# Performance work log

Measured on AMD Instinct MI355X. Metric: run time of the kernel, lower is better.

## Reference

```python
import jax, jax.numpy as jnp
import numpy as np

B, N, LATENT, HIDDEN = 65536, 32, 32, 64

def setup_inputs() -> dict:
    key = jax.random.key(0)
    ks = jax.random.split(key, 16)
    def xavier(k, shape):
        fan_in, fan_out = shape[1], shape[0]
        lim = float(np.sqrt(6.0 / (fan_in + fan_out)))
        return jax.random.uniform(k, shape, jnp.float32, -lim, lim)
    inp = {
        'x_sensors': jax.random.normal(ks[0], (B, N), jnp.float32),
        'state_x': jax.random.uniform(ks[1], (B, 1), jnp.float32),
        # GAT: W Linear(1, LATENT, bias=False), a Linear(2*LATENT, 1, bias=False), xavier init
        'W_gat': xavier(ks[2], (LATENT, 1)),
        'a_gat': xavier(ks[3], (1, 2 * LATENT)),
        # pooling: Linear(LATENT, LATENT//2) -> Tanh -> Linear(LATENT//2, 1) -> Softmax(dim=1)
        'p1_w': xavier(ks[4], (LATENT // 2, LATENT)),
        'p1_b': jnp.zeros((LATENT // 2,), jnp.float32),
        'p2_w': xavier(ks[5], (1, LATENT // 2)),
        'p2_b': jnp.zeros((1,), jnp.float32),
        # MNN: MonotonicLinear raw weights uniform(-0.5, 0.5), zero bias
        'm1_w': jax.random.uniform(ks[6], (HIDDEN, 1), jnp.float32, -0.5, 0.5),
        'm1_b': jnp.zeros((HIDDEN,), jnp.float32),
        'm2_w': jax.random.uniform(ks[7], (HIDDEN, HIDDEN), jnp.float32, -0.5, 0.5),
        'm2_b': jnp.zeros((HIDDEN,), jnp.float32),
        'm3_w': jax.random.uniform(ks[8], (LATENT, HIDDEN), jnp.float32, -0.5, 0.5),
        'm3_b': jnp.zeros((LATENT,), jnp.float32),
    }
    return inp

def reference(x_sensors, state_x, W_gat, a_gat, p1_w, p1_b, p2_w, p2_b,
              m1_w, m1_b, m2_w, m2_b, m3_w, m3_b):
    # --- GAT encoder ---
    # h = x_sensors[..., None] (B,N,1); Wh = h @ W_gat.T -> (B,N,D)
    Wh = jnp.einsum('bn,d->bnd', x_sensors, W_gat[:, 0])
    # e_ij = leakyrelu(a^T [Wh_i || Wh_j]) decomposed: a = [a1; a2]
    a1, a2 = a_gat[0, :LATENT], a_gat[0, LATENT:]
    s_i = jnp.einsum('bnd,d->bn', Wh, a1)  # contribution of Wh_i
    s_j = jnp.einsum('bnd,d->bn', Wh, a2)  # contribution of Wh_j
    e = jax.nn.leaky_relu(s_i[:, :, None] + s_j[:, None, :], 0.2)  # (B,N,N)
    alpha = jax.nn.softmax(e, axis=2)  # dropout is identity in eval
    h_prime = jnp.einsum('bij,bjd->bid', alpha, Wh)  # (B,N,D)
    # pooling: softmax over sensor dim (dim=1)
    t = jnp.tanh(h_prime @ p1_w.T + p1_b)
    beta = jax.nn.softmax(t @ p2_w.T + p2_b, axis=1)  # (B,N,1)
    z_enc = jnp.sum(h_prime * beta, axis=1)  # (B,D)
    # --- MNN decoder (exp-positive weights) ---
    h1 = jnp.tanh(state_x @ jnp.exp(m1_w).T + m1_b)
    h2 = jnp.tanh(h1 @ jnp.exp(m2_w).T + m2_b)
    z_dec = h2 @ jnp.exp(m3_w).T + m3_b  # (B,D)
    return (z_enc, z_dec)
```

## Files before the change

### kernel.cpp

```cpp
#include <hip/hip_runtime.h>
#include <hip/hip_bf16.h>

#define LOG2E     1.4426950408889634f
#define TWO_LOG2E 2.8853900817779268f

typedef __attribute__((ext_vector_type(8))) short    bf16x8;
typedef __attribute__((ext_vector_type(8))) _Float16 f16x8;
typedef __attribute__((ext_vector_type(4))) float    f32x4;
typedef __attribute__((ext_vector_type(2))) float    f32x2;

__device__ __forceinline__ float rcp_(float x){ return __builtin_amdgcn_rcpf(x); }
__device__ __forceinline__ float ex2_(float x){ return __builtin_amdgcn_exp2f(x); }

template<int K>
__device__ __forceinline__ float quadbc(float v){
  constexpr int ctrl = K * 0x55;
  return __int_as_float(__builtin_amdgcn_mov_dpp(__float_as_int(v), ctrl, 0xf, 0xf, true));
}

union FragB { bf16x8 v; uint32_t w[4]; uint4 u4; };
union FragH { f16x8  v; uint32_t w[4]; uint4 u4; };

__device__ __forceinline__ uint16_t f2bf(float x){
  union { __hip_bfloat16 h; uint16_t u; } c; c.h = __float2bfloat16(x); return c.u;
}
__device__ __forceinline__ float bf2f(uint16_t u){
  union { __hip_bfloat16 h; uint16_t u; } c; c.u = u; return __bfloat162float(c.h);
}
__device__ __forceinline__ uint32_t pkh(float a, float b){
  union { _Float16 h; uint16_t u; } ca, cb;
  ca.h = (_Float16)a; cb.h = (_Float16)b;
  return (uint32_t)ca.u | ((uint32_t)cb.u << 16);
}
__device__ __forceinline__ void split2(float a, float b, uint32_t& whi, uint32_t& wlo){
  uint16_t ah = f2bf(a), bh = f2bf(b);
  uint16_t al = f2bf(a - bf2f(ah)), bl_ = f2bf(b - bf2f(bh));
  whi = (uint32_t)ah | ((uint32_t)bh << 16);
  wlo = (uint32_t)al | ((uint32_t)bl_ << 16);
}
__device__ __forceinline__ void expsplit8(const float* __restrict__ src,
                                          FragB& hi, FragB& lo){
  float4 a = *(const float4*)src;
  float4 b = *(const float4*)(src + 4);
  float e0=__expf(a.x), e1=__expf(a.y), e2=__expf(a.z), e3=__expf(a.w);
  float e4=__expf(b.x), e5=__expf(b.y), e6=__expf(b.z), e7=__expf(b.w);
  split2(e0,e1, hi.w[0], lo.w[0]);
  split2(e2,e3, hi.w[1], lo.w[1]);
  split2(e4,e5, hi.w[2], lo.w[2]);
  split2(e6,e7, hi.w[3], lo.w[3]);
}
__device__ __forceinline__ void exph8(const float* __restrict__ src, FragH& out){
  float4 a = *(const float4*)src;
  float4 b = *(const float4*)(src + 4);
  out.w[0] = pkh(__expf(a.x), __expf(a.y));
  out.w[1] = pkh(__expf(a.z), __expf(a.w));
  out.w[2] = pkh(__expf(b.x), __expf(b.y));
  out.w[3] = pkh(__expf(b.z), __expf(b.w));
}

#define WS_FG1   0
#define WS_FG2H  2048
#define WS_FG2L  3072
#define WS_TBL   4096
#define WS_E1S   4608
#define WS_M1B   4672
#define WS_SCAL  4736

#define TBL_N     512
#define TBL_SCALE 25.6f
#define TBL_LO    -10.0f
#define TBL_CMAX  9.9f

__global__ __launch_bounds__(256) void IDSSM_pre(
    const float* __restrict__ Wg,  const float* __restrict__ ag,
    const float* __restrict__ p1w, const float* __restrict__ p1b,
    const float* __restrict__ p2w, const float* __restrict__ p2b,
    const float* __restrict__ m1w, const float* __restrict__ m1b,
    const float* __restrict__ m2w, const float* __restrict__ m3w,
    float* __restrict__ ws)
{
  const int blk = blockIdx.x;
  const int tid = threadIdx.x;
  const int l  = tid & 63;
  const int bl = l & 15, gt = l >> 4;
  if (blk < 2){
    const int s  = (blk*256 + tid) >> 6;
    const int mt = s >> 1, kt = s & 1;
    FragH h;
    exph8(m2w + (bl + 16*mt)*64 + 8*gt + 32*kt, h);
    *(uint4*)(ws + WS_FG1 + (size_t)(s*64 + l)*4) = h.u4;
  } else if (blk == 2){
    const int s2  = tid >> 6;
    const int mt2 = s2 >> 1, kt2 = s2 & 1;
    FragB hi, lo;
    expsplit8(m3w + (bl + 16*mt2)*64 + 8*gt + 32*kt2, hi, lo);
    *(uint4*)(ws + WS_FG2H + (size_t)(s2*64 + l)*4) = hi.u4;
    *(uint4*)(ws + WS_FG2L + (size_t)(s2*64 + l)*4) = lo.u4;
  } else if (blk == 3){
    __shared__ float qs[16], pb_[16], pw[16], u0s[1];
    if (tid < 16){
      float acc = 0.f;
      #pragma unroll
      for (int d = 0; d < 32; ++d) acc += p1w[tid*32 + d] * Wg[d];
      qs[tid]  = acc * TWO_LOG2E;
      pb_[tid] = p1b[tid] * TWO_LOG2E;
      pw[tid]  = -2.f * p2w[tid];
    }
    if (tid == 16){
      float sp = 0.f;
      #pragma unroll
      for (int k = 0; k < 16; ++k) sp += p2w[k];
      u0s[0] = sp + p2b[0];
    }
    __syncthreads();
    #pragma unroll
    for (int rep = 0; rep < 2; ++rep){
      const int n = tid + rep*256;
      const float c = TBL_LO + (float)n * (1.0f/TBL_SCALE);
      float u = u0s[0];
      #pragma unroll
      for (int k = 0; k < 16; ++k){
        float E = ex2_(fmaf(c, qs[k], pb_[k]));
        u = fmaf(pw[k], rcp_(E + 1.f), u);
      }
      ws[WS_TBL + n] = u * LOG2E;
    }
  } else {
    if (tid < 64){
      ws[WS_E1S + tid] = __expf(m1w[tid]) * TWO_LOG2E;
      ws[WS_M1B + tid] = m1b[tid] * TWO_LOG2E;
    } else if (tid == 64){
      float A1 = 0.f, A2 = 0.f;
      #pragma unroll
      for (int d = 0; d < 32; ++d){ A1 += Wg[d]*ag[d]; A2 += Wg[d]*ag[32+d]; }
      ws[WS_SCAL + 0] = A1 * LOG2E;
      ws[WS_SCAL + 1] = A2 * LOG2E;
    }
  }
}


#define EATT_J(SX, SF, SQ, JQ, JR) { \
    const float Fj_ = quadbc<JQ>(SF[JR]); \
    const float Fq_ = quadbc<JQ>(SQ[JR]); \
    const float xj_ = quadbc<JQ>(SX[JR]); \
    const f32x2 Fj2_ = {Fj_,Fj_}, Fq2_ = {Fq_,Fq_}, xj2_ = {xj_,xj_}; \
    f32x2 pe_; \
    pe_ = __builtin_elementwise_max(Ei2[0]*Fj2_, Eq2[0]*Fq2_); s2[0] = s2[0] + pe_; sx2[0] = sx2[0] + pe_*xj2_; \
    pe_ = __builtin_elementwise_max(Ei2[1]*Fj2_, Eq2[1]*Fq2_); s2[1] = s2[1] + pe_; sx2[1] = sx2[1] + pe_*xj2_; \
  }
#define EATT_Q(SX, SF, SQ, JQ) \
    EATT_J(SX,SF,SQ,JQ,0) EATT_J(SX,SF,SQ,JQ,1) EATT_J(SX,SF,SQ,JQ,2) EATT_J(SX,SF,SQ,JQ,3)
#define EATT_ALL(SX, SF, SQ) \
    EATT_Q(SX,SF,SQ,0) EATT_Q(SX,SF,SQ,1) EATT_Q(SX,SF,SQ,2) EATT_Q(SX,SF,SQ,3)

__global__ __launch_bounds__(256, 8) void IDSSM_enc(
    const float* __restrict__ xs, const float* __restrict__ Wg,
    const float* __restrict__ ws, float* __restrict__ out, int B)
{
  __shared__ float tbl[TBL_N];
  const int tid = threadIdx.x;
  const int lb  = tid >> 3;
  const int r   = tid & 7;
  const int b0  = blockIdx.x * 32;
  const int b   = b0 + lb;
  const bool valid = (b < B);
  const int rsrc = valid ? b : (B - 1);

  const float2 tco = *(const float2*)(ws + WS_TBL + tid*2);
  tbl[tid*2]     = tco.x;
  tbl[tid*2 + 1] = tco.y;

  const float A1p = ws[WS_SCAL + 0];
  const float A2p = ws[WS_SCAL + 1];

  const float4 xv = *(const float4*)(xs + (size_t)rsrc*32 + r*4);
  float xi[4] = { xv.x, xv.y, xv.z, xv.w };

  float Fjr[4], Fqr[4];
  #pragma unroll
  for (int t = 0; t < 4; ++t){
    const float tv = A2p * xi[t];
    Fjr[t] = ex2_(tv);
    Fqr[t] = ex2_(0.2f * tv);
  }
  float xo[4], Fo[4], Fqo[4];
  #pragma unroll
  for (int t = 0; t < 4; ++t){
    xo[t]  = __shfl_xor(xi[t], 4);
    Fo[t]  = __shfl_xor(Fjr[t], 4);
    Fqo[t] = __shfl_xor(Fqr[t], 4);
  }

  f32x2 Ei2[2], Eq2[2], s2[2], sx2[2];
  #pragma unroll
  for (int p = 0; p < 2; ++p){
    const float sa = A1p * xi[2*p], sb = A1p * xi[2*p + 1];
    Ei2[p] = (f32x2){ ex2_(sa), ex2_(sb) };
    Eq2[p] = (f32x2){ ex2_(0.2f*sa), ex2_(0.2f*sb) };
    s2[p]  = (f32x2)(0.f);
    sx2[p] = (f32x2)(0.f);
  }
  EATT_ALL(xi, Fjr, Fqr)
  EATT_ALL(xo, Fo,  Fqo)

  __syncthreads();

  float Zs = 0.f, Zd = 0.f;
  #pragma unroll
  for (int p = 0; p < 2; ++p){
    #pragma unroll
    for (int h = 0; h < 2; ++h){
      const float sv  = h ? s2[p].y  : s2[p].x;
      const float sxv = h ? sx2[p].y : sx2[p].x;
      const float c  = sxv * rcp_(sv);
      const float cc = fminf(fmaxf(c, TBL_LO), TBL_CMAX);
      const float f  = (cc - TBL_LO) * TBL_SCALE;
      const int   n  = (int)f;
      const float fr = f - (float)n;
      const float t0 = tbl[n];
      const float t1 = tbl[n + 1];
      const float eb = ex2_(fmaf(fr, t1 - t0, t0));
      Zs = fmaf(eb, c, Zs);
      Zd += eb;
    }
  }
  Zs += __shfl_xor(Zs, 1);  Zd += __shfl_xor(Zd, 1);
  Zs += __shfl_xor(Zs, 2);  Zd += __shfl_xor(Zd, 2);
  Zs += __shfl_xor(Zs, 4);  Zd += __shfl_xor(Zd, 4);
  const float Z = Zs * rcp_(Zd);

  if (valid){
    const float4 w = ((const float4*)Wg)[r];
    *(float4*)(out + (size_t)b*32 + r*4) =
        make_float4(Z*w.x, Z*w.y, Z*w.z, Z*w.w);
  }
}

__global__ __launch_bounds__(256, 4) void IDSSM_dec(
    const float* __restrict__ stx, const float* __restrict__ m2b,
    const float* __restrict__ m3b, const float* __restrict__ ws,
    float* __restrict__ out, int B)
{
  const int tid = threadIdx.x;
  const int b0  = blockIdx.x * 64;
  const int lane = tid & 63;
  const int wv   = tid >> 6;
  const int gt   = lane >> 4;
  const int bl   = lane & 15;
  const int bd   = b0 + wv*16 + bl;
  const float sx0 = stx[(bd < B) ? bd : (B-1)];

  uint4 fg1r[8];
  #pragma unroll
  for (int s = 0; s < 8; ++s)
    fg1r[s] = *(const uint4*)(ws + WS_FG1 + (size_t)(s*64 + lane)*4);

  FragH h1f[2];
  #pragma unroll
  for (int kt = 0; kt < 2; ++kt){
    const int g0 = 8*gt + 32*kt;
    const float4* e1p = (const float4*)(ws + WS_E1S + g0);
    const float4* m1p = (const float4*)(ws + WS_M1B + g0);
    float4 ea = e1p[0], eb4 = e1p[1];
    float4 ma = m1p[0], mb4 = m1p[1];
    float ev[8] = { ea.x,ea.y,ea.z,ea.w, eb4.x,eb4.y,eb4.z,eb4.w };
    float mv[8] = { ma.x,ma.y,ma.z,ma.w, mb4.x,mb4.y,mb4.z,mb4.w };
    float hv[8];
    #pragma unroll
    for (int j = 0; j < 8; ++j){
      float E = ex2_(fmaf(sx0, ev[j], mv[j]));
      hv[j] = fmaf(-2.f, rcp_(E + 1.f), 1.f);
    }
    #pragma unroll
    for (int jw = 0; jw < 4; ++jw)
      h1f[kt].w[jw] = pkh(hv[2*jw], hv[2*jw+1]);
  }

  f32x4 acc[4];
  #pragma unroll
  for (int mt = 0; mt < 4; ++mt){
    float4 bi = *(const float4*)(m2b + 16*mt + 4*gt);
    acc[mt][0]=bi.x; acc[mt][1]=bi.y; acc[mt][2]=bi.z; acc[mt][3]=bi.w;
  }
  #pragma unroll
  for (int mt = 0; mt < 4; ++mt){
    #pragma unroll
    for (int kt = 0; kt < 2; ++kt){
      FragH A; A.u4 = fg1r[mt*2 + kt];
      acc[mt] = __builtin_amdgcn_mfma_f32_16x16x32_f16(A.v, h1f[kt].v, acc[mt], 0, 0, 0);
    }
  }

  uint4 fg2h[4], fg2l[4];
  #pragma unroll
  for (int s = 0; s < 4; ++s){
    fg2h[s] = *(const uint4*)(ws + WS_FG2H + (size_t)(s*64 + lane)*4);
    fg2l[s] = *(const uint4*)(ws + WS_FG2L + (size_t)(s*64 + lane)*4);
  }

  uint32_t Whi[4][2], Wlo[4][2];
  #pragma unroll
  for (int mt = 0; mt < 4; ++mt){
    float t0 = fmaf(-2.f, rcp_(ex2_(acc[mt][0]*TWO_LOG2E) + 1.f), 1.f);
    float t1 = fmaf(-2.f, rcp_(ex2_(acc[mt][1]*TWO_LOG2E) + 1.f), 1.f);
    float t2 = fmaf(-2.f, rcp_(ex2_(acc[mt][2]*TWO_LOG2E) + 1.f), 1.f);
    float t3 = fmaf(-2.f, rcp_(ex2_(acc[mt][3]*TWO_LOG2E) + 1.f), 1.f);
    split2(t0, t1, Whi[mt][0], Wlo[mt][0]);
    split2(t2, t3, Whi[mt][1], Wlo[mt][1]);
  }

  FragB B2hi[2], B2lo[2];
  const int hiSel = gt >> 1;
  #pragma unroll
  for (int kt2 = 0; kt2 < 2; ++kt2){
    #pragma unroll
    for (int jw = 0; jw < 4; ++jw){
      const int sl = bl + 16*(((jw>>1) + 2*gt) & 3);
      const int w  = jw & 1;
      uint32_t c0 = (uint32_t)__shfl((int)Whi[2*kt2+0][w], sl);
      uint32_t c1 = (uint32_t)__shfl((int)Whi[2*kt2+1][w], sl);
      B2hi[kt2].w[jw] = hiSel ? c1 : c0;
      uint32_t d0 = (uint32_t)__shfl((int)Wlo[2*kt2+0][w], sl);
      uint32_t d1 = (uint32_t)__shfl((int)Wlo[2*kt2+1][w], sl);
      B2lo[kt2].w[jw] = hiSel ? d1 : d0;
    }
  }

  f32x4 acc2[2];
  #pragma unroll
  for (int mt2 = 0; mt2 < 2; ++mt2){
    float4 bi = *(const float4*)(m3b + 16*mt2 + 4*gt);
    acc2[mt2][0]=bi.x; acc2[mt2][1]=bi.y; acc2[mt2][2]=bi.z; acc2[mt2][3]=bi.w;
  }
  #pragma unroll
  for (int mt2 = 0; mt2 < 2; ++mt2){
    #pragma unroll
    for (int kt2 = 0; kt2 < 2; ++kt2){
      FragB Ahi, Alo;
      Ahi.u4 = fg2h[mt2*2 + kt2];
      Alo.u4 = fg2l[mt2*2 + kt2];
      acc2[mt2] = __builtin_amdgcn_mfma_f32_16x16x32_bf16(Ahi.v, B2hi[kt2].v, acc2[mt2], 0, 0, 0);
      acc2[mt2] = __builtin_amdgcn_mfma_f32_16x16x32_bf16(Ahi.v, B2lo[kt2].v, acc2[mt2], 0, 0, 0);
      acc2[mt2] = __builtin_amdgcn_mfma_f32_16x16x32_bf16(Alo.v, B2hi[kt2].v, acc2[mt2], 0, 0, 0);
    }
  }

  if (bd < B){
    float* o = out + (size_t)B*32 + (size_t)bd*32;
    *(float4*)(o + 4*gt)      = make_float4(acc2[0][0], acc2[0][1], acc2[0][2], acc2[0][3]);
    *(float4*)(o + 16 + 4*gt) = make_float4(acc2[1][0], acc2[1][1], acc2[1][2], acc2[1][3]);
  }
}

extern "C" void kernel_launch(void* const* d_in, const int* in_sizes, int n_in,
                              void* d_out, int out_size, void* d_ws, size_t ws_size,
                              hipStream_t stream)
{
  const float* xs  = (const float*)d_in[0];
  const float* stx = (const float*)d_in[1];
  const float* Wg  = (const float*)d_in[2];
  const float* ag  = (const float*)d_in[3];
  const float* p1w = (const float*)d_in[4];
  const float* p1b = (const float*)d_in[5];
  const float* p2w = (const float*)d_in[6];
  const float* p2b = (const float*)d_in[7];
  const float* m1w = (const float*)d_in[8];
  const float* m1b = (const float*)d_in[9];
  const float* m2w = (const float*)d_in[10];
  const float* m2b = (const float*)d_in[11];
  const float* m3w = (const float*)d_in[12];
  const float* m3b = (const float*)d_in[13];
  float* out = (float*)d_out;
  float* ws  = (float*)d_ws;
  const int B = in_sizes[0] / 32;

  hipLaunchKernelGGL(IDSSM_pre, dim3(5), dim3(256), 0, stream,
                     Wg, ag, p1w, p1b, p2w, p2b, m1w, m1b, m2w, m3w, ws);
  const int nbe = (B + 31) / 32;
  hipLaunchKernelGGL(IDSSM_enc, dim3(nbe), dim3(256), 0, stream,
                     xs, Wg, ws, out, B);
  const int nbd = (B + 63) / 64;
  hipLaunchKernelGGL(IDSSM_dec, dim3(nbd), dim3(256), 0, stream,
                     stx, m2b, m3b, ws, out, B);
}
```

Measured before the change: 28.50 us.

## Fuse encoder and decoder kernels and use single-pass fp16 MFMA for layer 3

Merges the separate encoder and decoder launches into one kernel. Each 32-row block runs the encoder with all four waves, then the first two waves run the decoder on the same rows. The third MNN layer drops the bf16 hi/lo split (three MFMAs per tile) for a single fp16 MFMA with fp16-packed exp weights and activations. This removes a kernel launch and most of the layer-3 matrix work. In exchange, half the waves sit idle during the decoder phase, occupancy is capped lower, and layer-3 accuracy drops to fp16.

```diff
diff --git a/kernel.cpp b/kernel.cpp
--- a/kernel.cpp
+++ b/kernel.cpp
@@ -4,7 +4,6 @@
 #define LOG2E     1.4426950408889634f
 #define TWO_LOG2E 2.8853900817779268f
 
-typedef __attribute__((ext_vector_type(8))) short    bf16x8;
 typedef __attribute__((ext_vector_type(8))) _Float16 f16x8;
 typedef __attribute__((ext_vector_type(4))) float    f32x4;
 typedef __attribute__((ext_vector_type(2))) float    f32x2;
@@ -18,36 +17,12 @@
   return __int_as_float(__builtin_amdgcn_mov_dpp(__float_as_int(v), ctrl, 0xf, 0xf, true));
 }
 
-union FragB { bf16x8 v; uint32_t w[4]; uint4 u4; };
-union FragH { f16x8  v; uint32_t w[4]; uint4 u4; };
-
-__device__ __forceinline__ uint16_t f2bf(float x){
-  union { __hip_bfloat16 h; uint16_t u; } c; c.h = __float2bfloat16(x); return c.u;
-}
-__device__ __forceinline__ float bf2f(uint16_t u){
-  union { __hip_bfloat16 h; uint16_t u; } c; c.u = u; return __bfloat162float(c.h);
-}
+union FragH { f16x8 v; uint32_t w[4]; uint4 u4; };
+
 __device__ __forceinline__ uint32_t pkh(float a, float b){
   union { _Float16 h; uint16_t u; } ca, cb;
   ca.h = (_Float16)a; cb.h = (_Float16)b;
   return (uint32_t)ca.u | ((uint32_t)cb.u << 16);
-}
-__device__ __forceinline__ void split2(float a, float b, uint32_t& whi, uint32_t& wlo){
-  uint16_t ah = f2bf(a), bh = f2bf(b);
-  uint16_t al = f2bf(a - bf2f(ah)), bl_ = f2bf(b - bf2f(bh));
-  whi = (uint32_t)ah | ((uint32_t)bh << 16);
-  wlo = (uint32_t)al | ((uint32_t)bl_ << 16);
-}
-__device__ __forceinline__ void expsplit8(const float* __restrict__ src,
-                                          FragB& hi, FragB& lo){
-  float4 a = *(const float4*)src;
-  float4 b = *(const float4*)(src + 4);
-  float e0=__expf(a.x), e1=__expf(a.y), e2=__expf(a.z), e3=__expf(a.w);
-  float e4=__expf(b.x), e5=__expf(b.y), e6=__expf(b.z), e7=__expf(b.w);
-  split2(e0,e1, hi.w[0], lo.w[0]);
-  split2(e2,e3, hi.w[1], lo.w[1]);
-  split2(e4,e5, hi.w[2], lo.w[2]);
-  split2(e6,e7, hi.w[3], lo.w[3]);
 }
 __device__ __forceinline__ void exph8(const float* __restrict__ src, FragH& out){
   float4 a = *(const float4*)src;
@@ -59,12 +34,11 @@
 }
 
 #define WS_FG1   0
-#define WS_FG2H  2048
-#define WS_FG2L  3072
-#define WS_TBL   4096
-#define WS_E1S   4608
-#define WS_M1B   4672
-#define WS_SCAL  4736
+#define WS_FG2   2048
+#define WS_TBL   3072
+#define WS_E1S   3584
+#define WS_M1B   3648
+#define WS_SCAL  3712
 
 #define TBL_N     512
 #define TBL_SCALE 25.6f
@@ -92,10 +66,9 @@
   } else if (blk == 2){
     const int s2  = tid >> 6;
     const int mt2 = s2 >> 1, kt2 = s2 & 1;
-    FragB hi, lo;
-    expsplit8(m3w + (bl + 16*mt2)*64 + 8*gt + 32*kt2, hi, lo);
-    *(uint4*)(ws + WS_FG2H + (size_t)(s2*64 + l)*4) = hi.u4;
-    *(uint4*)(ws + WS_FG2L + (size_t)(s2*64 + l)*4) = lo.u4;
+    FragH h;
+    exph8(m3w + (bl + 16*mt2)*64 + 8*gt + 32*kt2, h);
+    *(uint4*)(ws + WS_FG2 + (size_t)(s2*64 + l)*4) = h.u4;
   } else if (blk == 3){
     __shared__ float qs[16], pb_[16], pw[16], u0s[1];
     if (tid < 16){
@@ -139,7 +112,6 @@
   }
 }
 
-
 #define EATT_J(SX, SF, SQ, JQ, JR) { \
     const float Fj_ = quadbc<JQ>(SF[JR]); \
     const float Fq_ = quadbc<JQ>(SQ[JR]); \
@@ -154,9 +126,11 @@
 #define EATT_ALL(SX, SF, SQ) \
     EATT_Q(SX,SF,SQ,0) EATT_Q(SX,SF,SQ,1) EATT_Q(SX,SF,SQ,2) EATT_Q(SX,SF,SQ,3)
 
-__global__ __launch_bounds__(256, 8) void IDSSM_enc(
-    const float* __restrict__ xs, const float* __restrict__ Wg,
-    const float* __restrict__ ws, float* __restrict__ out, int B)
+__global__ __launch_bounds__(256, 6) void IDSSM_main(
+    const float* __restrict__ xs,  const float* __restrict__ stx,
+    const float* __restrict__ Wg,  const float* __restrict__ m2b,
+    const float* __restrict__ m3b, const float* __restrict__ ws,
+    float* __restrict__ out, int B)
 {
   __shared__ float tbl[TBL_N];
   const int tid = threadIdx.x;
@@ -235,17 +209,11 @@
     *(float4*)(out + (size_t)b*32 + r*4) =
         make_float4(Z*w.x, Z*w.y, Z*w.z, Z*w.w);
   }
-}
-
-__global__ __launch_bounds__(256, 4) void IDSSM_dec(
-    const float* __restrict__ stx, const float* __restrict__ m2b,
-    const float* __restrict__ m3b, const float* __restrict__ ws,
-    float* __restrict__ out, int B)
-{
-  const int tid = threadIdx.x;
-  const int b0  = blockIdx.x * 64;
+
+  const int wv = tid >> 6;
+  if (wv >= 2) return;
+
   const int lane = tid & 63;
-  const int wv   = tid >> 6;
   const int gt   = lane >> 4;
   const int bl   = lane & 15;
   const int bd   = b0 + wv*16 + bl;
@@ -292,25 +260,23 @@
     }
   }
 
-  uint4 fg2h[4], fg2l[4];
-  #pragma unroll
-  for (int s = 0; s < 4; ++s){
-    fg2h[s] = *(const uint4*)(ws + WS_FG2H + (size_t)(s*64 + lane)*4);
-    fg2l[s] = *(const uint4*)(ws + WS_FG2L + (size_t)(s*64 + lane)*4);
-  }
-
-  uint32_t Whi[4][2], Wlo[4][2];
+  uint4 fg2r[4];
+  #pragma unroll
+  for (int s = 0; s < 4; ++s)
+    fg2r[s] = *(const uint4*)(ws + WS_FG2 + (size_t)(s*64 + lane)*4);
+
+  uint32_t Wp[4][2];
   #pragma unroll
   for (int mt = 0; mt < 4; ++mt){
     float t0 = fmaf(-2.f, rcp_(ex2_(acc[mt][0]*TWO_LOG2E) + 1.f), 1.f);
     float t1 = fmaf(-2.f, rcp_(ex2_(acc[mt][1]*TWO_LOG2E) + 1.f), 1.f);
     float t2 = fmaf(-2.f, rcp_(ex2_(acc[mt][2]*TWO_LOG2E) + 1.f), 1.f);
     float t3 = fmaf(-2.f, rcp_(ex2_(acc[mt][3]*TWO_LOG2E) + 1.f), 1.f);
-    split2(t0, t1, Whi[mt][0], Wlo[mt][0]);
-    split2(t2, t3, Whi[mt][1], Wlo[mt][1]);
-  }
-
-  FragB B2hi[2], B2lo[2];
+    Wp[mt][0] = pkh(t0, t1);
+    Wp[mt][1] = pkh(t2, t3);
+  }
+
+  FragH B2[2];
   const int hiSel = gt >> 1;
   #pragma unroll
   for (int kt2 = 0; kt2 < 2; ++kt2){
@@ -318,12 +284,9 @@
     for (int jw = 0; jw < 4; ++jw){
       const int sl = bl + 16*(((jw>>1) + 2*gt) & 3);
       const int w  = jw & 1;
-      uint32_t c0 = (uint32_t)__shfl((int)Whi[2*kt2+0][w], sl);
-      uint32_t c1 = (uint32_t)__shfl((int)Whi[2*kt2+1][w], sl);
-      B2hi[kt2].w[jw] = hiSel ? c1 : c0;
-      uint32_t d0 = (uint32_t)__shfl((int)Wlo[2*kt2+0][w], sl);
-      uint32_t d1 = (uint32_t)__shfl((int)Wlo[2*kt2+1][w], sl);
-      B2lo[kt2].w[jw] = hiSel ? d1 : d0;
+      uint32_t c0 = (uint32_t)__shfl((int)Wp[2*kt2+0][w], sl);
+      uint32_t c1 = (uint32_t)__shfl((int)Wp[2*kt2+1][w], sl);
+      B2[kt2].w[jw] = hiSel ? c1 : c0;
     }
   }
 
@@ -337,12 +300,8 @@
   for (int mt2 = 0; mt2 < 2; ++mt2){
     #pragma unroll
     for (int kt2 = 0; kt2 < 2; ++kt2){
-      FragB Ahi, Alo;
-      Ahi.u4 = fg2h[mt2*2 + kt2];
-      Alo.u4 = fg2l[mt2*2 + kt2];
-      acc2[mt2] = __builtin_amdgcn_mfma_f32_16x16x32_bf16(Ahi.v, B2hi[kt2].v, acc2[mt2], 0, 0, 0);
-      acc2[mt2] = __builtin_amdgcn_mfma_f32_16x16x32_bf16(Ahi.v, B2lo[kt2].v, acc2[mt2], 0, 0, 0);
-      acc2[mt2] = __builtin_amdgcn_mfma_f32_16x16x32_bf16(Alo.v, B2hi[kt2].v, acc2[mt2], 0, 0, 0);
+      FragH A; A.u4 = fg2r[mt2*2 + kt2];
+      acc2[mt2] = __builtin_amdgcn_mfma_f32_16x16x32_f16(A.v, B2[kt2].v, acc2[mt2], 0, 0, 0);
     }
   }
 
@@ -377,10 +336,7 @@
 
   hipLaunchKernelGGL(IDSSM_pre, dim3(5), dim3(256), 0, stream,
                      Wg, ag, p1w, p1b, p2w, p2b, m1w, m1b, m2w, m3w, ws);
-  const int nbe = (B + 31) / 32;
-  hipLaunchKernelGGL(IDSSM_enc, dim3(nbe), dim3(256), 0, stream,
-                     xs, Wg, ws, out, B);
-  const int nbd = (B + 63) / 64;
-  hipLaunchKernelGGL(IDSSM_dec, dim3(nbd), dim3(256), 0, stream,
-                     stx, m2b, m3b, ws, out, B);
-}
+  const int nblk = (B + 31) / 32;
+  hipLaunchKernelGGL(IDSSM_main, dim3(nblk), dim3(256), 0, stream,
+                     xs, stx, Wg, m2b, m3b, ws, out, B);
+}
```

After: 26.95 us. 1.06x faster.
